# Performance work log

Measured on AMD Instinct MI355X. Metric: run time of the kernel, lower is better.

Reference implementation:

```python
import jax, jax.numpy as jnp
import numpy as np

B, S, D_IN, D = 4, 4096, 768, 64

def setup_inputs() -> dict:
    key = jax.random.key(0)
    kx, kq, kk, kv = jax.random.split(key, 4)
    std = 0.02
    return {
        "x": jax.random.normal(kx, (B, S, D_IN), dtype=jnp.float32),
        "wq": jax.random.normal(kq, (D_IN, D), dtype=jnp.float32) * std,
        "wk": jax.random.normal(kk, (D_IN, D), dtype=jnp.float32) * std,
        "wv": jax.random.normal(kv, (D_IN, D), dtype=jnp.float32) * std,
    }

def reference(x, wq, wk, wv):
    # q,k,v: [B,S,d]
    q = jnp.einsum('bsi,id->bsd', x, wq)
    k = jnp.einsum('bsi,id->bsd', x, wk)
    v = jnp.einsum('bsi,id->bsd', x, wv)
    scale = 1.0 / np.sqrt(q.shape[-1]).astype(np.float32)
    scores = jnp.einsum('bqd,bkd->bqk', q, k) * scale  # [B,S,S]
    attn = jax.nn.softmax(scores, axis=-1)
    return jnp.einsum('bqk,bkd->bqd', attn, v)  # [B,S,d]
```

## Files before the change

### kernel.cpp

```cpp
#include <hip/hip_runtime.h>
#include <hip/hip_bf16.h>

#define B_   4
#define S_   4096
#define DIN  768
#define DH   64

typedef float f32x4 __attribute__((ext_vector_type(4)));
typedef short s16x8 __attribute__((ext_vector_type(8)));
typedef unsigned short u16;

__device__ __forceinline__ u16 f2bf(float f) {
  union { float f; unsigned int u; } a; a.f = f;
  unsigned int u = a.u;
  unsigned int r = (u + 0x7fffu + ((u >> 16) & 1u)) >> 16;
  return (u16)r;
}

__device__ __forceinline__ s16x8 ld8s(const u16* p) {
  return *reinterpret_cast<const s16x8*>(p);
}

__device__ __forceinline__ s16x8 pack8(float4 a, float4 b) {
  s16x8 h;
  h[0] = (short)f2bf(a.x); h[1] = (short)f2bf(a.y);
  h[2] = (short)f2bf(a.z); h[3] = (short)f2bf(a.w);
  h[4] = (short)f2bf(b.x); h[5] = (short)f2bf(b.y);
  h[6] = (short)f2bf(b.z); h[7] = (short)f2bf(b.w);
  return h;
}

#define GLD_LDS(gp, lp) \
  __builtin_amdgcn_global_load_lds((const __attribute__((address_space(1))) void*)(gp), \
                                   (__attribute__((address_space(3))) void*)(lp), 16, 0, 0)

__global__ void prep_w(const float* __restrict__ wq, const float* __restrict__ wk,
                       const float* __restrict__ wv, u16* __restrict__ wt) {
  int tid = blockIdx.x * 256 + threadIdx.x;
  if (tid >= 192 * DIN) return;
  int n = tid / DIN, k = tid % DIN;
  const float* src; float scale = 1.0f; int col;
  if (n < 64)       { src = wq; col = n;       scale = 0.125f; }
  else if (n < 128) { src = wk; col = n - 64;  }
  else              { src = wv; col = n - 128; }
  float v = src[k * DH + col] * scale;
  int chunk = k & ~63;
  int kin = k & 63;
  int gr = (kin >> 3) ^ (n & 7);
  wt[n * DIN + chunk + gr * 8 + (kin & 7)] = f2bf(v);
}

__global__ __launch_bounds__(256) void qkv_gemm(const float* __restrict__ x,
    const u16* __restrict__ wt, u16* __restrict__ qb, u16* __restrict__ kb,
    u16* __restrict__ vt) {
  __shared__ __align__(16) u16 xl[2][32 * 72];
  __shared__ __align__(16) u16 wl[2][192 * 64];
  int t = threadIdx.x;
  int w = t >> 6, l = t & 63, g = l >> 4, lq = l & 15;
  int wr = w >> 1, wc = w & 1;
  int m0 = blockIdx.x * 32;
  int xrow = t >> 3, xc = t & 7;

  f32x4 acc[6];
#pragma unroll
  for (int i = 0; i < 6; i++) acc[i] = f32x4{0.f, 0.f, 0.f, 0.f};

  const float* xp0 = x + (size_t)(m0 + xrow) * DIN + xc * 8;

  {
    float4 xa = *reinterpret_cast<const float4*>(xp0);
    float4 xb = *reinterpret_cast<const float4*>(xp0 + 4);
#pragma unroll
    for (int i = 0; i < 6; i++) {
      int tau = i * 4 + w; int n = 8 * tau + (l >> 3);
      GLD_LDS(wt + n * DIN + (l & 7) * 8, &wl[0][tau * 512]);
    }
    *reinterpret_cast<s16x8*>(&xl[0][xrow * 72 + xc * 8]) = pack8(xa, xb);
    asm volatile("s_waitcnt vmcnt(0)" ::: "memory");
    __syncthreads();
  }

  for (int ks = 0; ks < 12; ks++) {
    int cur = ks & 1;
    bool more = ks < 11;
    float4 na, nb;
    if (more) {
      int k1 = (ks + 1) * 64;
      na = *reinterpret_cast<const float4*>(xp0 + k1);
      nb = *reinterpret_cast<const float4*>(xp0 + k1 + 4);
#pragma unroll
      for (int i = 0; i < 6; i++) {
        int tau = i * 4 + w; int n = 8 * tau + (l >> 3);
        GLD_LDS(wt + n * DIN + k1 + (l & 7) * 8, &wl[cur ^ 1][tau * 512]);
      }
    }
    s16x8 a0 = ld8s(&xl[cur][(16 * wr + lq) * 72 + g * 8]);
    s16x8 a1 = ld8s(&xl[cur][(16 * wr + lq) * 72 + g * 8 + 32]);
#pragma unroll
    for (int nt = 0; nt < 6; nt++) {
      int n = wc * 96 + nt * 16 + lq;
      s16x8 b0 = ld8s(&wl[cur][n * 64 + ((g ^ (n & 7)) * 8)]);
      s16x8 b1 = ld8s(&wl[cur][n * 64 + (((g + 4) ^ (n & 7)) * 8)]);
      acc[nt] = __builtin_amdgcn_mfma_f32_16x16x32_bf16(a0, b0, acc[nt], 0, 0, 0);
      acc[nt] = __builtin_amdgcn_mfma_f32_16x16x32_bf16(a1, b1, acc[nt], 0, 0, 0);
    }
    if (more) {
      asm volatile("s_waitcnt vmcnt(0)" ::: "memory");
      *reinterpret_cast<s16x8*>(&xl[cur ^ 1][xrow * 72 + xc * 8]) = pack8(na, nb);
      __syncthreads();
    }
  }

  int b = m0 >> 12;
  int srow0 = (m0 & (S_ - 1)) + 16 * wr + 4 * g;
#pragma unroll
  for (int nt = 0; nt < 6; nt++) {
    int col = wc * 96 + nt * 16 + lq;
    u16* base; int c;
    if (col < 64)       { base = qb; c = col; }
    else if (col < 128) { base = kb; c = col - 64; }
    else                { base = vt; c = col - 128; }
#pragma unroll
    for (int r = 0; r < 4; r++) {
      int srow = srow0 + r;
      u16 hv = f2bf(acc[nt][r]);
      if (col < 128) {
        int gr = (c >> 3) ^ (srow & 7);
        base[(size_t)(b * S_ + srow) * DH + gr * 8 + (c & 7)] = hv;
      } else {
        int gr = ((srow >> 3) & 7) ^ (c & 7);
        base[(size_t)(b * DH + c) * S_ + (srow & ~63) + gr * 8 + (srow & 7)] = hv;
      }
    }
  }
}

__global__ __launch_bounds__(512) void attn(const u16* __restrict__ qb,
    const u16* __restrict__ kb, const u16* __restrict__ vt, float* __restrict__ out) {
  __shared__ __align__(16) u16 smem[41984];

  int t = threadIdx.x;
  int w8 = t >> 6, half = w8 >> 2, w = w8 & 3, l = t & 63, g = l >> 4, lq = l & 15;
  int bq = blockIdx.x;
  int b = bq >> 6;
  int q0 = (bq & 63) * 64;
  int kvbase = half * 2048;

  int sq = q0 + 16 * w + lq;
  const u16* qrow = qb + (size_t)(b * S_ + sq) * DH;
  s16x8 qa0 = ld8s(qrow + ((g ^ (sq & 7)) * 8));
  s16x8 qa1 = ld8s(qrow + (((g + 4) ^ (sq & 7)) * 8));

  u16* pl = smem + 32768 + w8 * 1152;

  float mrun[4], lrun[4];
  f32x4 acco[4];
#pragma unroll
  for (int r = 0; r < 4; r++) { mrun[r] = -1e30f; lrun[r] = 0.f; }
#pragma unroll
  for (int nt = 0; nt < 4; nt++) acco[nt] = f32x4{0.f, 0.f, 0.f, 0.f};

  int tau0 = w * 2;
  int srow_st = 8 * tau0 + (l >> 3);
  int gcol = (l & 7) * 8;

  {
    u16* dst = smem + half * 16384;
#pragma unroll
    for (int i = 0; i < 2; i++) {
      int row = srow_st + 8 * i;
      GLD_LDS(kb + (size_t)(b * S_ + kvbase + row) * DH + gcol, &dst[(tau0 + i) * 512]);
      GLD_LDS(vt + (size_t)(b * DH + row) * S_ + kvbase + gcol, &dst[4096 + (tau0 + i) * 512]);
    }
    asm volatile("s_waitcnt vmcnt(0)" ::: "memory");
    __syncthreads();
  }

  for (int it = 0; it < 32; it++) {
    int cur = it & 1;
    bool more = it < 31;
    if (more) {
      int k1 = kvbase + (it + 1) * 64;
      u16* dst = smem + half * 16384 + (cur ^ 1) * 8192;
#pragma unroll
      for (int i = 0; i < 2; i++) {
        int row = srow_st + 8 * i;
        GLD_LDS(kb + (size_t)(b * S_ + k1 + row) * DH + gcol, &dst[(tau0 + i) * 512]);
        GLD_LDS(vt + (size_t)(b * DH + row) * S_ + k1 + gcol, &dst[4096 + (tau0 + i) * 512]);
      }
    }
    const u16* kl = smem + half * 16384 + cur * 8192;
    const u16* vl = kl + 4096;

    f32x4 accs[4];
#pragma unroll
    for (int kt = 0; kt < 4; kt++) {
      int krow = kt * 16 + lq;
      s16x8 kf0 = ld8s(&kl[krow * 64 + ((g ^ (krow & 7)) * 8)]);
      s16x8 kf1 = ld8s(&kl[krow * 64 + (((g + 4) ^ (krow & 7)) * 8)]);
      f32x4 c = f32x4{0.f, 0.f, 0.f, 0.f};
      c = __builtin_amdgcn_mfma_f32_16x16x32_bf16(qa0, kf0, c, 0, 0, 0);
      c = __builtin_amdgcn_mfma_f32_16x16x32_bf16(qa1, kf1, c, 0, 0, 0);
      accs[kt] = c;
    }

    float p[4][4];
    float scale[4];
#pragma unroll
    for (int r = 0; r < 4; r++) {
      float mx = fmaxf(fmaxf(accs[0][r], accs[1][r]), fmaxf(accs[2][r], accs[3][r]));
      mx = fmaxf(mx, __shfl_xor(mx, 1));
      mx = fmaxf(mx, __shfl_xor(mx, 2));
      mx = fmaxf(mx, __shfl_xor(mx, 4));
      mx = fmaxf(mx, __shfl_xor(mx, 8));
      float mnew = fmaxf(mrun[r], mx);
      scale[r] = exp2f((mrun[r] - mnew) * 1.44269504f);
      float s = 0.f;
#pragma unroll
      for (int kt = 0; kt < 4; kt++) {
        float pv = exp2f((accs[kt][r] - mnew) * 1.44269504f);
        p[kt][r] = pv; s += pv;
      }
      s += __shfl_xor(s, 1); s += __shfl_xor(s, 2);
      s += __shfl_xor(s, 4); s += __shfl_xor(s, 8);
      lrun[r] = lrun[r] * scale[r] + s;
      mrun[r] = mnew;
    }

#pragma unroll
    for (int kt = 0; kt < 4; kt++)
#pragma unroll
      for (int r = 0; r < 4; r++)
        pl[(4 * g + r) * 72 + kt * 16 + lq] = f2bf(p[kt][r]);
    asm volatile("s_waitcnt lgkmcnt(0)" ::: "memory");

#pragma unroll
    for (int nt = 0; nt < 4; nt++)
#pragma unroll
      for (int r = 0; r < 4; r++)
        acco[nt][r] *= scale[r];

    s16x8 pa0 = ld8s(&pl[lq * 72 + g * 8]);
    s16x8 pa1 = ld8s(&pl[lq * 72 + g * 8 + 32]);
#pragma unroll
    for (int nt = 0; nt < 4; nt++) {
      int d = nt * 16 + lq;
      s16x8 vf0 = ld8s(&vl[d * 64 + ((g ^ (d & 7)) * 8)]);
      s16x8 vf1 = ld8s(&vl[d * 64 + (((g + 4) ^ (d & 7)) * 8)]);
      acco[nt] = __builtin_amdgcn_mfma_f32_16x16x32_bf16(pa0, vf0, acco[nt], 0, 0, 0);
      acco[nt] = __builtin_amdgcn_mfma_f32_16x16x32_bf16(pa1, vf1, acco[nt], 0, 0, 0);
    }
    if (more) {
      asm volatile("s_waitcnt vmcnt(0)" ::: "memory");
      __syncthreads();
    }
  }

  __syncthreads();
  float* mO = reinterpret_cast<float*>(smem);
  float* mM = reinterpret_cast<float*>(smem) + 4096;
  float* mL = mM + 64;

  if (half == 1) {
#pragma unroll
    for (int nt = 0; nt < 4; nt++)
#pragma unroll
      for (int r = 0; r < 4; r++)
        mO[(16 * w + 4 * g + r) * 64 + nt * 16 + lq] = acco[nt][r];
    if (lq == 0) {
#pragma unroll
      for (int r = 0; r < 4; r++) {
        int row = 16 * w + 4 * g + r;
        mM[row] = mrun[r];
        mL[row] = lrun[r];
      }
    }
  }
  __syncthreads();
  if (half == 0) {
#pragma unroll
    for (int r = 0; r < 4; r++) {
      int row = 16 * w + 4 * g + r;
      float m2 = mM[row], l2 = mL[row];
      float m = fmaxf(mrun[r], m2);
      float f1 = exp2f((mrun[r] - m) * 1.44269504f);
      float f2 = exp2f((m2 - m) * 1.44269504f);
      float inv = 1.0f / (lrun[r] * f1 + l2 * f2);
#pragma unroll
      for (int nt = 0; nt < 4; nt++) {
        float val = (acco[nt][r] * f1 + mO[row * 64 + nt * 16 + lq] * f2) * inv;
        out[(size_t)(b * S_ + q0 + row) * DH + nt * 16 + lq] = val;
      }
    }
  }
}

extern "C" void kernel_launch(void* const* d_in, const int* in_sizes, int n_in,
                              void* d_out, int out_size, void* d_ws, size_t ws_size,
                              hipStream_t stream) {
  const float* x  = (const float*)d_in[0];
  const float* wq = (const float*)d_in[1];
  const float* wk = (const float*)d_in[2];
  const float* wv = (const float*)d_in[3];
  float* out = (float*)d_out;
  char* ws = (char*)d_ws;

  u16* wt = (u16*)(ws);
  u16* qb = (u16*)(ws + 294912);
  u16* kb = (u16*)(ws + 294912 + 2097152);
  u16* vt = (u16*)(ws + 294912 + 2 * 2097152);

  hipLaunchKernelGGL(prep_w,   dim3(576), dim3(256), 0, stream, wq, wk, wv, wt);
  hipLaunchKernelGGL(qkv_gemm, dim3(512), dim3(256), 0, stream, x, wt, qb, kb, vt);
  hipLaunchKernelGGL(attn,     dim3(256), dim3(512), 0, stream, qb, kb, vt, out);
}
```

Before: 169.0 us.

## Transpose QK^T MFMA so each lane owns one query row for softmax

Swaps the MFMA operand order so the score tile is S^T, giving each lane a single query row. The row max and sum then need two cross-group shuffles instead of four shuffles per row for each of four rows, and running max/sum become scalars. P is written to LDS as packed 8-byte bf16 stores using a cheaper round-half-up conversion instead of 16 scalar u16 stores. This adds a few shuffles to broadcast the rescale factors back to the output layout, and slightly changes bf16 rounding of P.

```diff
diff --git a/kernel.cpp b/kernel.cpp
--- a/kernel.cpp
+++ b/kernel.cpp
@@ -15,6 +15,11 @@
   unsigned int u = a.u;
   unsigned int r = (u + 0x7fffu + ((u >> 16) & 1u)) >> 16;
   return (u16)r;
+}
+
+__device__ __forceinline__ unsigned int bfpack2(float a, float b) {
+  union { float f; unsigned int u; } ua, ub; ua.f = a; ub.f = b;
+  return ((ua.u + 0x8000u) >> 16) | ((ub.u + 0x8000u) & 0xffff0000u);
 }
 
 __device__ __forceinline__ s16x8 ld8s(const u16* p) {
@@ -153,10 +158,8 @@
 
   u16* pl = smem + 32768 + w8 * 1152;
 
-  float mrun[4], lrun[4];
+  float mrun = -1e30f, lrun = 0.f;
   f32x4 acco[4];
-#pragma unroll
-  for (int r = 0; r < 4; r++) { mrun[r] = -1e30f; lrun[r] = 0.f; }
 #pragma unroll
   for (int nt = 0; nt < 4; nt++) acco[nt] = f32x4{0.f, 0.f, 0.f, 0.f};
 
@@ -175,6 +178,8 @@
     asm volatile("s_waitcnt vmcnt(0)" ::: "memory");
     __syncthreads();
   }
+
+  const float L2E = 1.44269504f;
 
   for (int it = 0; it < 32; it++) {
     int cur = it & 1;
@@ -199,49 +204,56 @@
       s16x8 kf0 = ld8s(&kl[krow * 64 + ((g ^ (krow & 7)) * 8)]);
       s16x8 kf1 = ld8s(&kl[krow * 64 + (((g + 4) ^ (krow & 7)) * 8)]);
       f32x4 c = f32x4{0.f, 0.f, 0.f, 0.f};
-      c = __builtin_amdgcn_mfma_f32_16x16x32_bf16(qa0, kf0, c, 0, 0, 0);
-      c = __builtin_amdgcn_mfma_f32_16x16x32_bf16(qa1, kf1, c, 0, 0, 0);
+      c = __builtin_amdgcn_mfma_f32_16x16x32_bf16(kf0, qa0, c, 0, 0, 0);
+      c = __builtin_amdgcn_mfma_f32_16x16x32_bf16(kf1, qa1, c, 0, 0, 0);
       accs[kt] = c;
     }
 
-    float p[4][4];
-    float scale[4];
-#pragma unroll
-    for (int r = 0; r < 4; r++) {
-      float mx = fmaxf(fmaxf(accs[0][r], accs[1][r]), fmaxf(accs[2][r], accs[3][r]));
-      mx = fmaxf(mx, __shfl_xor(mx, 1));
-      mx = fmaxf(mx, __shfl_xor(mx, 2));
-      mx = fmaxf(mx, __shfl_xor(mx, 4));
-      mx = fmaxf(mx, __shfl_xor(mx, 8));
-      float mnew = fmaxf(mrun[r], mx);
-      scale[r] = exp2f((mrun[r] - mnew) * 1.44269504f);
-      float s = 0.f;
-#pragma unroll
-      for (int kt = 0; kt < 4; kt++) {
-        float pv = exp2f((accs[kt][r] - mnew) * 1.44269504f);
-        p[kt][r] = pv; s += pv;
-      }
-      s += __shfl_xor(s, 1); s += __shfl_xor(s, 2);
-      s += __shfl_xor(s, 4); s += __shfl_xor(s, 8);
-      lrun[r] = lrun[r] * scale[r] + s;
-      mrun[r] = mnew;
-    }
-
-#pragma unroll
-    for (int kt = 0; kt < 4; kt++)
-#pragma unroll
-      for (int r = 0; r < 4; r++)
-        pl[(4 * g + r) * 72 + kt * 16 + lq] = f2bf(p[kt][r]);
+    float mx = fmaxf(fmaxf(accs[0][0], accs[0][1]), fmaxf(accs[0][2], accs[0][3]));
+#pragma unroll
+    for (int kt = 1; kt < 4; kt++)
+      mx = fmaxf(mx, fmaxf(fmaxf(accs[kt][0], accs[kt][1]),
+                           fmaxf(accs[kt][2], accs[kt][3])));
+    mx = fmaxf(mx, __shfl_xor(mx, 16));
+    mx = fmaxf(mx, __shfl_xor(mx, 32));
+    float mnew = fmaxf(mrun, mx);
+    float scale = exp2f((mrun - mnew) * L2E);
+    float sc0 = __shfl(scale, 4 * g + 0);
+    float sc1 = __shfl(scale, 4 * g + 1);
+    float sc2 = __shfl(scale, 4 * g + 2);
+    float sc3 = __shfl(scale, 4 * g + 3);
+
+    float s = 0.f;
+#pragma unroll
+    for (int kt = 0; kt < 4; kt++) {
+#pragma unroll
+      for (int r = 0; r < 4; r++) {
+        float e = exp2f((accs[kt][r] - mnew) * L2E);
+        accs[kt][r] = e; s += e;
+      }
+    }
+    s += __shfl_xor(s, 16);
+    s += __shfl_xor(s, 32);
+    lrun = lrun * scale + s;
+    mrun = mnew;
+
+#pragma unroll
+    for (int kt = 0; kt < 4; kt++) {
+      uint2 u;
+      u.x = bfpack2(accs[kt][0], accs[kt][1]);
+      u.y = bfpack2(accs[kt][2], accs[kt][3]);
+      *reinterpret_cast<uint2*>(&pl[lq * 72 + kt * 16 + 4 * g]) = u;
+    }
     asm volatile("s_waitcnt lgkmcnt(0)" ::: "memory");
 
 #pragma unroll
-    for (int nt = 0; nt < 4; nt++)
-#pragma unroll
-      for (int r = 0; r < 4; r++)
-        acco[nt][r] *= scale[r];
+    for (int nt = 0; nt < 4; nt++) {
+      acco[nt][0] *= sc0; acco[nt][1] *= sc1;
+      acco[nt][2] *= sc2; acco[nt][3] *= sc3;
+    }
 
     s16x8 pa0 = ld8s(&pl[lq * 72 + g * 8]);
-    s16x8 pa1 = ld8s(&pl[lq * 72 + g * 8 + 32]);
+    s16x8 pa1 = ld8s(&pl[lq * 72 + 32 + g * 8]);
 #pragma unroll
     for (int nt = 0; nt < 4; nt++) {
       int d = nt * 16 + lq;
@@ -267,13 +279,9 @@
 #pragma unroll
       for (int r = 0; r < 4; r++)
         mO[(16 * w + 4 * g + r) * 64 + nt * 16 + lq] = acco[nt][r];
-    if (lq == 0) {
-#pragma unroll
-      for (int r = 0; r < 4; r++) {
-        int row = 16 * w + 4 * g + r;
-        mM[row] = mrun[r];
-        mL[row] = lrun[r];
-      }
+    if (g == 0) {
+      mM[16 * w + lq] = mrun;
+      mL[16 * w + lq] = lrun;
     }
   }
   __syncthreads();
@@ -281,11 +289,13 @@
 #pragma unroll
     for (int r = 0; r < 4; r++) {
       int row = 16 * w + 4 * g + r;
+      float m1 = __shfl(mrun, 4 * g + r);
+      float l1 = __shfl(lrun, 4 * g + r);
       float m2 = mM[row], l2 = mL[row];
-      float m = fmaxf(mrun[r], m2);
-      float f1 = exp2f((mrun[r] - m) * 1.44269504f);
+      float m = fmaxf(m1, m2);
+      float f1 = exp2f((m1 - m) * 1.44269504f);
       float f2 = exp2f((m2 - m) * 1.44269504f);
-      float inv = 1.0f / (lrun[r] * f1 + l2 * f2);
+      float inv = 1.0f / (l1 * f1 + l2 * f2);
 #pragma unroll
       for (int nt = 0; nt < 4; nt++) {
         float val = (acco[nt][r] * f1 + mO[row * 64 + nt * 16 + lq] * f2) * inv;
```

Result: faster. 150.2 us (-11.1%).
